# Performance work log

Hardware: AMD Instinct MI355X
Metric: run time of the kernel (lower is better)

The kernel has to match this reference:

```python
import jax, jax.numpy as jnp
import numpy as np

T, B = 256, 512
IMG_FLAT = 25          # 5*5*num_channels
FEAT = 16; LOC = 4; EMB = 4
LSTM_IN = FEAT + LOC + EMB  # 24
H = 128
GRID = 10.0


def _lin(k, out_d, in_d, scale=0.05):
    kw, kb = jax.random.split(k)
    return (jax.random.normal(kw, (out_d, in_d), jnp.float32) * scale,
            jax.random.normal(kb, (out_d,), jnp.float32) * scale)


def setup_inputs() -> dict:
    key = jax.random.key(0)
    ks = jax.random.split(key, 16)
    image = jax.random.uniform(ks[0], (T * B, 5, 5), jnp.float32) * 255.0
    location = jax.random.uniform(ks[1], (T * B, 2), jnp.float32) * GRID
    message = jax.random.normal(ks[2], (T * B, 1), jnp.float32)
    done = jax.random.randint(ks[3], (T * B,), 0, 2, jnp.int32)
    h0 = jnp.zeros((1, B, H), jnp.float32)
    c0 = jnp.zeros((1, B, H), jnp.float32)
    Wv1, bv1 = _lin(ks[4], 256, IMG_FLAT)
    Wv2, bv2 = _lin(ks[5], 256, 256)
    Wv3, bv3 = _lin(ks[6], 128, 256)
    Wv4, bv4 = _lin(ks[7], FEAT, 128)
    Wl, bl = _lin(ks[8], LOC, 2)
    Wm, bm = _lin(ks[9], EMB, 1)
    Wih, bih = _lin(ks[10], 4 * H, LSTM_IN)
    Whh, bhh = _lin(ks[11], 4 * H, H)
    return dict(image=image, location=location, message=message, done=done,
                h0=h0, c0=c0,
                Wv1=Wv1, bv1=bv1, Wv2=Wv2, bv2=bv2, Wv3=Wv3, bv3=bv3,
                Wv4=Wv4, bv4=bv4, Wl=Wl, bl=bl, Wm=Wm, bm=bm,
                Wih=Wih, bih=bih, Whh=Whh, bhh=bhh)


def _get_states(image, location, message, done_f, h0, c0,
                Wv1, bv1, Wv2, bv2, Wv3, bv3, Wv4, bv4,
                Wl, bl, Wm, bm, Wih, bih, Whh, bhh):
    batch = h0.shape[1]
    # encoders (all rows at once, faithful to torch version)
    x = image.reshape(image.shape[0], -1) / 255.0
    f = jax.nn.relu(x @ Wv1.T + bv1)
    f = jax.nn.relu(f @ Wv2.T + bv2)
    f = jax.nn.relu(f @ Wv3.T + bv3)
    image_feat = jax.nn.relu(f @ Wv4.T + bv4)                  # [TB, 16]
    loc_feat = (location / GRID) @ Wl.T + bl                    # [TB, 4]
    msg = (1.0 - done_f)[:, None] * message
    msg_feat = jax.nn.relu(msg @ Wm.T + bm)                     # [TB, 4]
    hid = jnp.concatenate([image_feat, loc_feat, msg_feat], axis=1)
    hid = hid.reshape(-1, batch, LSTM_IN)                       # [T, B, 24]
    d_seq = done_f.reshape(-1, batch)                           # [T, B]

    def step(carry, xd):
        h, c = carry
        x_t, d_t = xd
        mask = (1.0 - d_t)[:, None]
        h = h * mask
        c = c * mask
        gates = x_t @ Wih.T + bih + h @ Whh.T + bhh             # [B, 4H]
        i, fg, g, o = jnp.split(gates, 4, axis=-1)
        c = jax.nn.sigmoid(fg) * c + jax.nn.sigmoid(i) * jnp.tanh(g)
        h = jax.nn.sigmoid(o) * jnp.tanh(c)
        return (h, c), h

    (hT, cT), hs = jax.lax.scan(step, (h0[0], c0[0]), (hid, d_seq))
    new_hidden = hs.reshape(-1, H)                              # [TB, 128]
    return new_hidden, hT[None], cT[None]


def reference(image, location, message, done, h0, c0,
              Wv1, bv1, Wv2, bv2, Wv3, bv3, Wv4, bv4,
              Wl, bl, Wm, bm, Wih, bih, Whh, bhh):
    done_f = done.astype(jnp.float32)
    return _get_states(image, location, message, done_f, h0, c0,
                       Wv1, bv1, Wv2, bv2, Wv3, bv3, Wv4, bv4,
                       Wl, bl, Wm, bm, Wih, bih, Whh, bhh)
```

## Files before the change

kernel.cpp:

```cpp
#include <hip/hip_runtime.h>
#include <hip/hip_bf16.h>

#define T_STEPS 256
#define BATCH   512
#define HID     128
#define TBROWS  (T_STEPS * BATCH)
#define XH_STRIDE 32

typedef short  bh8   __attribute__((ext_vector_type(8)));
typedef _Float16 h8  __attribute__((ext_vector_type(8)));
typedef float  f32x4 __attribute__((ext_vector_type(4)));

__device__ __forceinline__ unsigned short f2bf_bits(float x) {
    union { float f; unsigned int u; } a; a.f = x;
    unsigned int r = a.u + 0x7fffu + ((a.u >> 16) & 1u);
    return (unsigned short)(r >> 16);
}
__device__ __forceinline__ unsigned short f2h_bits(float x) {
    union { _Float16 h; unsigned short u; } z; z.h = (_Float16)x; return z.u;
}
__device__ __forceinline__ unsigned int pack2h(float a, float b) {
    union { _Float16 h[2]; unsigned int u; } z;
    z.h[0] = (_Float16)a; z.h[1] = (_Float16)b; return z.u;
}

#if __has_builtin(__builtin_amdgcn_rcpf)
__device__ __forceinline__ float frcp(float x) { return __builtin_amdgcn_rcpf(x); }
#else
__device__ __forceinline__ float frcp(float x) { return 1.0f / x; }
#endif
#if __has_builtin(__builtin_amdgcn_exp2f)
__device__ __forceinline__ float fexp2(float x) { return __builtin_amdgcn_exp2f(x); }
#else
__device__ __forceinline__ float fexp2(float x) { return __expf(x * 0.6931471806f); }
#endif
#define LOG2E 1.442695041f
__device__ __forceinline__ float sigf(float x) {
    return frcp(1.0f + fexp2(-x * LOG2E));
}
__device__ __forceinline__ float tanh_fast(float x) {
    return fmaf(-2.0f, frcp(1.0f + fexp2(x * (2.0f * LOG2E))), 1.0f);
}

__device__ __forceinline__ void fragstore(unsigned short* dst, const float* W,
                                          int i, int NT, int Kreal) {
    const int j    = i & 7;
    const int lane = (i >> 3) & 63;
    const int ts   = i >> 9;
    const int nt   = ts % NT;
    const int ks   = ts / NT;
    const int n = nt * 16 + (lane & 15);
    const int k = ks * 32 + (lane >> 4) * 8 + j;
    dst[i] = (k < Kreal) ? f2bf_bits(W[n * Kreal + k]) : (unsigned short)0;
}

#define NE1 8192
#define NE2 65536
#define NE3 32768
#define NE4 2048
#define NWC 81920
#define NBS 512
#define PREP_TOTAL (NE1 + NE2 + NE3 + NE4 + NWC + NBS)

__global__ __launch_bounds__(256) void prep_kernel(
    const float* __restrict__ W1, const float* __restrict__ W2,
    const float* __restrict__ W3, const float* __restrict__ W4,
    const float* __restrict__ Wih, const float* __restrict__ bih,
    const float* __restrict__ Whh, const float* __restrict__ bhh,
    unsigned short* __restrict__ w1f, unsigned short* __restrict__ w2f,
    unsigned short* __restrict__ w3f, unsigned short* __restrict__ w4f,
    unsigned short* __restrict__ wcf, float* __restrict__ bsum)
{
    int i = blockIdx.x * 256 + threadIdx.x;
    if (i < NE1) { fragstore(w1f, W1, i, 16, 25); return; }
    i -= NE1;
    if (i < NE2) { fragstore(w2f, W2, i, 16, 256); return; }
    i -= NE2;
    if (i < NE3) { fragstore(w3f, W3, i, 8, 256); return; }
    i -= NE3;
    if (i < NE4) { fragstore(w4f, W4, i, 1, 128); return; }
    i -= NE4;
    if (i < NWC) {
        const int j    = i & 7;
        const int lane = (i >> 3) & 63;
        const int ts   = i >> 9;
        const int mt   = ts / 5;
        const int kt   = ts - mt * 5;
        const int m = mt * 16 + (lane & 15);
        const int k = kt * 32 + (lane >> 4) * 8 + j;
        float v = 0.0f;
        if (k < 128)      v = Whh[m * 128 + k];
        else if (k < 152) v = Wih[m * 24 + (k - 128)];
        wcf[i] = f2h_bits(v);
        return;
    }
    i -= NWC;
    if (i < NBS) bsum[i] = bih[i] + bhh[i];
}

#define ASTRIDE 264

__global__ __launch_bounds__(256) void encoder_kernel(
    const float* __restrict__ img,
    const float* __restrict__ loc,
    const float* __restrict__ msg,
    const int*   __restrict__ done,
    const float* __restrict__ B1, const float* __restrict__ B2,
    const float* __restrict__ B3, const float* __restrict__ B4,
    const float* __restrict__ Wl, const float* __restrict__ Bl,
    const float* __restrict__ Wm, const float* __restrict__ Bm,
    const unsigned short* __restrict__ w1f, const unsigned short* __restrict__ w2f,
    const unsigned short* __restrict__ w3f, const unsigned short* __restrict__ w4f,
    unsigned short* __restrict__ xcat_h)
{
    __shared__ unsigned short actA[4][16][ASTRIDE];
    __shared__ unsigned short actB[4][16][ASTRIDE];

    const int tid  = threadIdx.x;
    const int w    = tid >> 6;
    const int lane = tid & 63;
    const int m    = lane & 15;
    const int quad = lane >> 4;
    const int wrow0 = blockIdx.x * 64 + w * 16;

    if (tid < 64) {
        const int grow = blockIdx.x * 64 + tid;
        const float l0 = loc[grow * 2 + 0] * 0.1f;
        const float l1 = loc[grow * 2 + 1] * 0.1f;
        #pragma unroll
        for (int c = 0; c < 4; ++c)
            xcat_h[grow * XH_STRIDE + 16 + c] =
                f2h_bits(fmaf(Wl[c * 2 + 0], l0, fmaf(Wl[c * 2 + 1], l1, Bl[c])));
        const float mm = (1.0f - (float)done[grow]) * msg[grow];
        #pragma unroll
        for (int c = 0; c < 4; ++c)
            xcat_h[grow * XH_STRIDE + 20 + c] =
                f2h_bits(fmaxf(fmaf(Wm[c], mm, Bm[c]), 0.0f));
    }

    const f32x4 zero4 = {0.0f, 0.0f, 0.0f, 0.0f};

    {
        bh8 af;
        const int grow = wrow0 + m;
        #pragma unroll
        for (int j = 0; j < 8; ++j) {
            const int k = quad * 8 + j;
            const float v = (k < 25) ? img[grow * 25 + k] * (1.0f / 255.0f) : 0.0f;
            af[j] = (short)f2bf_bits(v);
        }
        f32x4 acc[16];
        #pragma unroll
        for (int nt = 0; nt < 16; ++nt) {
            const bh8 bf_ = *reinterpret_cast<const bh8*>(w1f + (nt * 64 + lane) * 8);
            acc[nt] = __builtin_amdgcn_mfma_f32_16x16x32_bf16(af, bf_, zero4, 0, 0, 0);
        }
        #pragma unroll
        for (int nt = 0; nt < 16; ++nt) {
            const float bb = B1[nt * 16 + m];
            #pragma unroll
            for (int r = 0; r < 4; ++r)
                actA[w][quad * 4 + r][nt * 16 + m] = f2bf_bits(fmaxf(acc[nt][r] + bb, 0.0f));
        }
    }

    {
        f32x4 acc[16];
        #pragma unroll
        for (int nt = 0; nt < 16; ++nt) acc[nt] = zero4;
        #pragma unroll
        for (int ks = 0; ks < 8; ++ks) {
            const bh8 af = *reinterpret_cast<const bh8*>(&actA[w][m][ks * 32 + quad * 8]);
            const unsigned short* wp = w2f + ((ks * 16) * 64 + lane) * 8;
            #pragma unroll
            for (int nt = 0; nt < 16; ++nt) {
                const bh8 bf_ = *reinterpret_cast<const bh8*>(wp + nt * 512);
                acc[nt] = __builtin_amdgcn_mfma_f32_16x16x32_bf16(af, bf_, acc[nt], 0, 0, 0);
            }
        }
        #pragma unroll
        for (int nt = 0; nt < 16; ++nt) {
            const float bb = B2[nt * 16 + m];
            #pragma unroll
            for (int r = 0; r < 4; ++r)
                actB[w][quad * 4 + r][nt * 16 + m] = f2bf_bits(fmaxf(acc[nt][r] + bb, 0.0f));
        }
    }

    {
        f32x4 acc[8];
        #pragma unroll
        for (int nt = 0; nt < 8; ++nt) acc[nt] = zero4;
        #pragma unroll
        for (int ks = 0; ks < 8; ++ks) {
            const bh8 af = *reinterpret_cast<const bh8*>(&actB[w][m][ks * 32 + quad * 8]);
            const unsigned short* wp = w3f + ((ks * 8) * 64 + lane) * 8;
            #pragma unroll
            for (int nt = 0; nt < 8; ++nt) {
                const bh8 bf_ = *reinterpret_cast<const bh8*>(wp + nt * 512);
                acc[nt] = __builtin_amdgcn_mfma_f32_16x16x32_bf16(af, bf_, acc[nt], 0, 0, 0);
            }
        }
        #pragma unroll
        for (int nt = 0; nt < 8; ++nt) {
            const float bb = B3[nt * 16 + m];
            #pragma unroll
            for (int r = 0; r < 4; ++r)
                actA[w][quad * 4 + r][nt * 16 + m] = f2bf_bits(fmaxf(acc[nt][r] + bb, 0.0f));
        }
    }

    {
        f32x4 acc = zero4;
        #pragma unroll
        for (int ks = 0; ks < 4; ++ks) {
            const bh8 af = *reinterpret_cast<const bh8*>(&actA[w][m][ks * 32 + quad * 8]);
            const bh8 bf_ = *reinterpret_cast<const bh8*>(w4f + (ks * 64 + lane) * 8);
            acc = __builtin_amdgcn_mfma_f32_16x16x32_bf16(af, bf_, acc, 0, 0, 0);
        }
        const float bb = B4[m];
        #pragma unroll
        for (int r = 0; r < 4; ++r) {
            const int grow = wrow0 + quad * 4 + r;
            xcat_h[grow * XH_STRIDE + m] = f2h_bits(fmaxf(acc[r] + bb, 0.0f));
        }
    }
}

#define HXS 168

__global__ __launch_bounds__(512, 2) void lstm_kernel(
    const unsigned short* __restrict__ xcat_h,
    const int*   __restrict__ done,
    const float* __restrict__ h0,
    const float* __restrict__ c0,
    const unsigned short* __restrict__ wcf,
    const float* __restrict__ bsum,
    float* __restrict__ out)
{
    __shared__ unsigned short hx[2][16][HXS];

    const int tid  = threadIdx.x;
    const int w    = tid >> 6;
    const int lane = tid & 63;
    const int n    = lane & 15;
    const int quad = lane >> 4;
    const int bb   = blockIdx.x * 16;
    const int u0   = w * 16 + quad * 4;

    h8 wf[4][5];
    #pragma unroll
    for (int g = 0; g < 4; ++g)
        #pragma unroll
        for (int kt = 0; kt < 5; ++kt)
            wf[g][kt] = *reinterpret_cast<const h8*>(
                wcf + (size_t)(((g * 8 + w) * 5 + kt) * 64 + lane) * 8);

    float bi[4][4];
    #pragma unroll
    for (int g = 0; g < 4; ++g)
        #pragma unroll
        for (int r = 0; r < 4; ++r)
            bi[g][r] = bsum[g * 128 + u0 + r];

    float c_[4];
    {
        const float4 cv = *reinterpret_cast<const float4*>(c0 + (size_t)(bb + n) * HID + u0);
        c_[0] = cv.x; c_[1] = cv.y; c_[2] = cv.z; c_[3] = cv.w;
    }

    if (tid < 128) {
        const int b_ = tid >> 6, r_ = (tid >> 2) & 15, j_ = tid & 3;
        *reinterpret_cast<unsigned int*>(&hx[b_][r_][152 + 2 * j_]) = 0u;
    }
    for (int i = tid; i < 16 * HID; i += 512) {
        const int nn = i >> 7, uu = i & 127;
        const float m0 = 1.0f - (float)done[bb + nn];
        hx[0][nn][uu] = f2h_bits(h0[(size_t)(bb + nn) * HID + uu] * m0);
    }
    if (tid < 192) {
        const int nl = tid / 12, kp = tid - nl * 12;
        const unsigned int v = *reinterpret_cast<const unsigned int*>(
            xcat_h + (size_t)(bb + nl) * XH_STRIDE + 2 * kp);
        *reinterpret_cast<unsigned int*>(&hx[0][nl][128 + 2 * kp]) = v;
    }
    int mc_i = done[bb + n];
    int mn_i = done[BATCH + bb + n];
    __syncthreads();

    float hn[4] = {0.0f, 0.0f, 0.0f, 0.0f};

    #pragma unroll 2
    for (int s = 0; s < T_STEPS; ++s) {
        const int buf = s & 1, nbuf = buf ^ 1;

        h8 bf[5];
        #pragma unroll
        for (int kt = 0; kt < 5; ++kt)
            bf[kt] = *reinterpret_cast<const h8*>(&hx[buf][n][kt * 32 + quad * 8]);

        unsigned int xreg = 0;
        if (tid < 192) {
            const int nl = tid / 12, kp = tid - nl * 12;
            const int rowx = (s + 1 < T_STEPS ? s + 1 : T_STEPS - 1) * BATCH + bb + nl;
            xreg = *reinterpret_cast<const unsigned int*>(
                xcat_h + (size_t)rowx * XH_STRIDE + 2 * kp);
        }
        const int mf_i = done[(s + 2 < T_STEPS ? s + 2 : T_STEPS - 1) * BATCH + bb + n];

        f32x4 acc[4];
        #pragma unroll
        for (int g = 0; g < 4; ++g) {
            acc[g][0] = bi[g][0]; acc[g][1] = bi[g][1];
            acc[g][2] = bi[g][2]; acc[g][3] = bi[g][3];
        }
        #pragma unroll
        for (int kt = 0; kt < 5; ++kt)
            #pragma unroll
            for (int g = 0; g < 4; ++g)
                acc[g] = __builtin_amdgcn_mfma_f32_16x16x32_f16(wf[g][kt], bf[kt], acc[g], 0, 0, 0);

        const float mcur = 1.0f - (float)mc_i;
        const float mnxt = 1.0f - (float)mn_i;
        #pragma unroll
        for (int r = 0; r < 4; ++r) {
            const float gi = acc[0][r], gf = acc[1][r];
            const float gg = acc[2][r], go = acc[3][r];
            const float cn = sigf(gf) * (c_[r] * mcur) + sigf(gi) * tanh_fast(gg);
            hn[r] = sigf(go) * tanh_fast(cn);
            c_[r] = cn;
        }

        const int row = s * BATCH + bb + n;
        float4 ov; ov.x = hn[0]; ov.y = hn[1]; ov.z = hn[2]; ov.w = hn[3];
        *reinterpret_cast<float4*>(out + (size_t)row * HID + u0) = ov;

        *reinterpret_cast<unsigned int*>(&hx[nbuf][n][u0])     = pack2h(hn[0] * mnxt, hn[1] * mnxt);
        *reinterpret_cast<unsigned int*>(&hx[nbuf][n][u0 + 2]) = pack2h(hn[2] * mnxt, hn[3] * mnxt);
        if (tid < 192) {
            const int nl = tid / 12, kp = tid - nl * 12;
            *reinterpret_cast<unsigned int*>(&hx[nbuf][nl][128 + 2 * kp]) = xreg;
        }
        mc_i = mn_i; mn_i = mf_i;
        __syncthreads();
    }

    const size_t base = (size_t)TBROWS * HID;
    float4 hv; hv.x = hn[0]; hv.y = hn[1]; hv.z = hn[2]; hv.w = hn[3];
    *reinterpret_cast<float4*>(out + base + (size_t)(bb + n) * HID + u0) = hv;
    float4 cvo; cvo.x = c_[0]; cvo.y = c_[1]; cvo.z = c_[2]; cvo.w = c_[3];
    *reinterpret_cast<float4*>(out + base + (size_t)BATCH * HID + (size_t)(bb + n) * HID + u0) = cvo;
}

extern "C" void kernel_launch(void* const* d_in, const int* in_sizes, int n_in,
                              void* d_out, int out_size, void* d_ws, size_t ws_size,
                              hipStream_t stream) {
    const float* img  = (const float*)d_in[0];
    const float* loc  = (const float*)d_in[1];
    const float* msg  = (const float*)d_in[2];
    const int*   done = (const int*)d_in[3];
    const float* h0   = (const float*)d_in[4];
    const float* c0   = (const float*)d_in[5];
    const float* W1   = (const float*)d_in[6];
    const float* B1   = (const float*)d_in[7];
    const float* W2   = (const float*)d_in[8];
    const float* B2   = (const float*)d_in[9];
    const float* W3   = (const float*)d_in[10];
    const float* B3   = (const float*)d_in[11];
    const float* W4   = (const float*)d_in[12];
    const float* B4   = (const float*)d_in[13];
    const float* Wl   = (const float*)d_in[14];
    const float* Bl   = (const float*)d_in[15];
    const float* Wm   = (const float*)d_in[16];
    const float* Bm   = (const float*)d_in[17];
    const float* Wih  = (const float*)d_in[18];
    const float* bih  = (const float*)d_in[19];
    const float* Whh  = (const float*)d_in[20];
    const float* bhh  = (const float*)d_in[21];

    char* wsb = (char*)d_ws;
    unsigned short* xcat_h = (unsigned short*)wsb;
    unsigned short* w1f = (unsigned short*)(wsb + (size_t)TBROWS * XH_STRIDE * 2);
    unsigned short* w2f = w1f + NE1;
    unsigned short* w3f = w2f + NE2;
    unsigned short* w4f = w3f + NE3;
    unsigned short* wcf = w4f + NE4;
    float*          bsum = (float*)(wcf + NWC);

    float* out = (float*)d_out;

    prep_kernel<<<(PREP_TOTAL + 255) / 256, 256, 0, stream>>>(
        W1, W2, W3, W4, Wih, bih, Whh, bhh,
        w1f, w2f, w3f, w4f, wcf, bsum);
    encoder_kernel<<<TBROWS / 64, 256, 0, stream>>>(
        img, loc, msg, done, B1, B2, B3, B4, Wl, Bl, Wm, Bm,
        w1f, w2f, w3f, w4f, xcat_h);
    lstm_kernel<<<BATCH / 16, 512, 0, stream>>>(
        xcat_h, done, h0, c0, wcf, bsum, out);
}
```

Baseline: 413.3 us.

## Transpose encoder MFMAs to 32 rows per wave and split LSTM into 2-column blocks

```diff
diff --git a/kernel.cpp b/kernel.cpp
--- a/kernel.cpp
+++ b/kernel.cpp
@@ -22,6 +22,9 @@
 __device__ __forceinline__ unsigned int pack2h(float a, float b) {
     union { _Float16 h[2]; unsigned int u; } z;
     z.h[0] = (_Float16)a; z.h[1] = (_Float16)b; return z.u;
+}
+__device__ __forceinline__ unsigned int pack2bf(float a, float b) {
+    return (unsigned int)f2bf_bits(a) | ((unsigned int)f2bf_bits(b) << 16);
 }
 
 #if __has_builtin(__builtin_amdgcn_rcpf)
@@ -113,123 +116,160 @@
     const unsigned short* __restrict__ w3f, const unsigned short* __restrict__ w4f,
     unsigned short* __restrict__ xcat_h)
 {
-    __shared__ unsigned short actA[4][16][ASTRIDE];
-    __shared__ unsigned short actB[4][16][ASTRIDE];
+    __shared__ __align__(16) unsigned short actA[4][32][ASTRIDE];
+    __shared__ __align__(16) unsigned short actB[4][32][ASTRIDE];
 
     const int tid  = threadIdx.x;
     const int w    = tid >> 6;
     const int lane = tid & 63;
-    const int m    = lane & 15;
+    const int n    = lane & 15;
     const int quad = lane >> 4;
-    const int wrow0 = blockIdx.x * 64 + w * 16;
-
-    if (tid < 64) {
-        const int grow = blockIdx.x * 64 + tid;
-        const float l0 = loc[grow * 2 + 0] * 0.1f;
-        const float l1 = loc[grow * 2 + 1] * 0.1f;
+    const int wrow0 = blockIdx.x * 128 + w * 32;
+
+    if (tid < 128) {
+        const int grow = blockIdx.x * 128 + tid;
+        const float l0 = loc[(size_t)grow * 2 + 0] * 0.1f;
+        const float l1 = loc[(size_t)grow * 2 + 1] * 0.1f;
         #pragma unroll
         for (int c = 0; c < 4; ++c)
-            xcat_h[grow * XH_STRIDE + 16 + c] =
+            xcat_h[(size_t)grow * XH_STRIDE + 16 + c] =
                 f2h_bits(fmaf(Wl[c * 2 + 0], l0, fmaf(Wl[c * 2 + 1], l1, Bl[c])));
         const float mm = (1.0f - (float)done[grow]) * msg[grow];
         #pragma unroll
         for (int c = 0; c < 4; ++c)
-            xcat_h[grow * XH_STRIDE + 20 + c] =
+            xcat_h[(size_t)grow * XH_STRIDE + 20 + c] =
                 f2h_bits(fmaxf(fmaf(Wm[c], mm, Bm[c]), 0.0f));
     }
 
     const f32x4 zero4 = {0.0f, 0.0f, 0.0f, 0.0f};
 
     {
-        bh8 af;
-        const int grow = wrow0 + m;
-        #pragma unroll
-        for (int j = 0; j < 8; ++j) {
-            const int k = quad * 8 + j;
-            const float v = (k < 25) ? img[grow * 25 + k] * (1.0f / 255.0f) : 0.0f;
-            af[j] = (short)f2bf_bits(v);
-        }
-        f32x4 acc[16];
-        #pragma unroll
-        for (int nt = 0; nt < 16; ++nt) {
-            const bh8 bf_ = *reinterpret_cast<const bh8*>(w1f + (nt * 64 + lane) * 8);
-            acc[nt] = __builtin_amdgcn_mfma_f32_16x16x32_bf16(af, bf_, zero4, 0, 0, 0);
-        }
-        #pragma unroll
-        for (int nt = 0; nt < 16; ++nt) {
-            const float bb = B1[nt * 16 + m];
-            #pragma unroll
-            for (int r = 0; r < 4; ++r)
-                actA[w][quad * 4 + r][nt * 16 + m] = f2bf_bits(fmaxf(acc[nt][r] + bb, 0.0f));
-        }
-    }
+        bh8 bimg[2];
+        #pragma unroll
+        for (int sg = 0; sg < 2; ++sg) {
+            const size_t grow = wrow0 + sg * 16 + n;
+            #pragma unroll
+            for (int j = 0; j < 8; ++j) {
+                const int k = quad * 8 + j;
+                const float v = (k < 25) ? img[grow * 25 + k] * (1.0f / 255.0f) : 0.0f;
+                bimg[sg][j] = (short)f2bf_bits(v);
+            }
+        }
+        f32x4 a1[16][2];
+        #pragma unroll
+        for (int mt = 0; mt < 16; ++mt) {
+            const bh8 a = *reinterpret_cast<const bh8*>(w1f + (size_t)(mt * 64 + lane) * 8);
+            a1[mt][0] = __builtin_amdgcn_mfma_f32_16x16x32_bf16(a, bimg[0], zero4, 0, 0, 0);
+            a1[mt][1] = __builtin_amdgcn_mfma_f32_16x16x32_bf16(a, bimg[1], zero4, 0, 0, 0);
+        }
+        #pragma unroll
+        for (int mt = 0; mt < 16; ++mt) {
+            const float4 bv = *reinterpret_cast<const float4*>(B1 + mt * 16 + quad * 4);
+            #pragma unroll
+            for (int sg = 0; sg < 2; ++sg) {
+                const float v0 = fmaxf(a1[mt][sg][0] + bv.x, 0.0f);
+                const float v1 = fmaxf(a1[mt][sg][1] + bv.y, 0.0f);
+                const float v2 = fmaxf(a1[mt][sg][2] + bv.z, 0.0f);
+                const float v3 = fmaxf(a1[mt][sg][3] + bv.w, 0.0f);
+                uint2 pk; pk.x = pack2bf(v0, v1); pk.y = pack2bf(v2, v3);
+                *reinterpret_cast<uint2*>(&actA[w][sg * 16 + n][mt * 16 + quad * 4]) = pk;
+            }
+        }
+    }
+    __syncthreads();
 
     {
-        f32x4 acc[16];
-        #pragma unroll
-        for (int nt = 0; nt < 16; ++nt) acc[nt] = zero4;
-        #pragma unroll
-        for (int ks = 0; ks < 8; ++ks) {
-            const bh8 af = *reinterpret_cast<const bh8*>(&actA[w][m][ks * 32 + quad * 8]);
-            const unsigned short* wp = w2f + ((ks * 16) * 64 + lane) * 8;
-            #pragma unroll
-            for (int nt = 0; nt < 16; ++nt) {
-                const bh8 bf_ = *reinterpret_cast<const bh8*>(wp + nt * 512);
-                acc[nt] = __builtin_amdgcn_mfma_f32_16x16x32_bf16(af, bf_, acc[nt], 0, 0, 0);
-            }
-        }
-        #pragma unroll
-        for (int nt = 0; nt < 16; ++nt) {
-            const float bb = B2[nt * 16 + m];
-            #pragma unroll
-            for (int r = 0; r < 4; ++r)
-                actB[w][quad * 4 + r][nt * 16 + m] = f2bf_bits(fmaxf(acc[nt][r] + bb, 0.0f));
-        }
-    }
+        f32x4 a2[16][2];
+        #pragma unroll
+        for (int mt = 0; mt < 16; ++mt) { a2[mt][0] = zero4; a2[mt][1] = zero4; }
+        #pragma unroll
+        for (int kt = 0; kt < 8; ++kt) {
+            const bh8 b0 = *reinterpret_cast<const bh8*>(&actA[w][n][kt * 32 + quad * 8]);
+            const bh8 b1 = *reinterpret_cast<const bh8*>(&actA[w][16 + n][kt * 32 + quad * 8]);
+            #pragma unroll
+            for (int mt = 0; mt < 16; ++mt) {
+                const bh8 a = *reinterpret_cast<const bh8*>(
+                    w2f + (size_t)((kt * 16 + mt) * 64 + lane) * 8);
+                a2[mt][0] = __builtin_amdgcn_mfma_f32_16x16x32_bf16(a, b0, a2[mt][0], 0, 0, 0);
+                a2[mt][1] = __builtin_amdgcn_mfma_f32_16x16x32_bf16(a, b1, a2[mt][1], 0, 0, 0);
+            }
+        }
+        #pragma unroll
+        for (int mt = 0; mt < 16; ++mt) {
+            const float4 bv = *reinterpret_cast<const float4*>(B2 + mt * 16 + quad * 4);
+            #pragma unroll
+            for (int sg = 0; sg < 2; ++sg) {
+                const float v0 = fmaxf(a2[mt][sg][0] + bv.x, 0.0f);
+                const float v1 = fmaxf(a2[mt][sg][1] + bv.y, 0.0f);
+                const float v2 = fmaxf(a2[mt][sg][2] + bv.z, 0.0f);
+                const float v3 = fmaxf(a2[mt][sg][3] + bv.w, 0.0f);
+                uint2 pk; pk.x = pack2bf(v0, v1); pk.y = pack2bf(v2, v3);
+                *reinterpret_cast<uint2*>(&actB[w][sg * 16 + n][mt * 16 + quad * 4]) = pk;
+            }
+        }
+    }
+    __syncthreads();
 
     {
-        f32x4 acc[8];
-        #pragma unroll
-        for (int nt = 0; nt < 8; ++nt) acc[nt] = zero4;
-        #pragma unroll
-        for (int ks = 0; ks < 8; ++ks) {
-            const bh8 af = *reinterpret_cast<const bh8*>(&actB[w][m][ks * 32 + quad * 8]);
-            const unsigned short* wp = w3f + ((ks * 8) * 64 + lane) * 8;
-            #pragma unroll
-            for (int nt = 0; nt < 8; ++nt) {
-                const bh8 bf_ = *reinterpret_cast<const bh8*>(wp + nt * 512);
-                acc[nt] = __builtin_amdgcn_mfma_f32_16x16x32_bf16(af, bf_, acc[nt], 0, 0, 0);
-            }
-        }
-        #pragma unroll
-        for (int nt = 0; nt < 8; ++nt) {
-            const float bb = B3[nt * 16 + m];
-            #pragma unroll
-            for (int r = 0; r < 4; ++r)
-                actA[w][quad * 4 + r][nt * 16 + m] = f2bf_bits(fmaxf(acc[nt][r] + bb, 0.0f));
-        }
-    }
+        f32x4 a3[8][2];
+        #pragma unroll
+        for (int mt = 0; mt < 8; ++mt) { a3[mt][0] = zero4; a3[mt][1] = zero4; }
+        #pragma unroll
+        for (int kt = 0; kt < 8; ++kt) {
+            const bh8 b0 = *reinterpret_cast<const bh8*>(&actB[w][n][kt * 32 + quad * 8]);
+            const bh8 b1 = *reinterpret_cast<const bh8*>(&actB[w][16 + n][kt * 32 + quad * 8]);
+            #pragma unroll
+            for (int mt = 0; mt < 8; ++mt) {
+                const bh8 a = *reinterpret_cast<const bh8*>(
+                    w3f + (size_t)((kt * 8 + mt) * 64 + lane) * 8);
+                a3[mt][0] = __builtin_amdgcn_mfma_f32_16x16x32_bf16(a, b0, a3[mt][0], 0, 0, 0);
+                a3[mt][1] = __builtin_amdgcn_mfma_f32_16x16x32_bf16(a, b1, a3[mt][1], 0, 0, 0);
+            }
+        }
+        #pragma unroll
+        for (int mt = 0; mt < 8; ++mt) {
+            const float4 bv = *reinterpret_cast<const float4*>(B3 + mt * 16 + quad * 4);
+            #pragma unroll
+            for (int sg = 0; sg < 2; ++sg) {
+                const float v0 = fmaxf(a3[mt][sg][0] + bv.x, 0.0f);
+                const float v1 = fmaxf(a3[mt][sg][1] + bv.y, 0.0f);
+                const float v2 = fmaxf(a3[mt][sg][2] + bv.z, 0.0f);
+                const float v3 = fmaxf(a3[mt][sg][3] + bv.w, 0.0f);
+                uint2 pk; pk.x = pack2bf(v0, v1); pk.y = pack2bf(v2, v3);
+                *reinterpret_cast<uint2*>(&actA[w][sg * 16 + n][mt * 16 + quad * 4]) = pk;
+            }
+        }
+    }
+    __syncthreads();
 
     {
-        f32x4 acc = zero4;
-        #pragma unroll
-        for (int ks = 0; ks < 4; ++ks) {
-            const bh8 af = *reinterpret_cast<const bh8*>(&actA[w][m][ks * 32 + quad * 8]);
-            const bh8 bf_ = *reinterpret_cast<const bh8*>(w4f + (ks * 64 + lane) * 8);
-            acc = __builtin_amdgcn_mfma_f32_16x16x32_bf16(af, bf_, acc, 0, 0, 0);
-        }
-        const float bb = B4[m];
-        #pragma unroll
-        for (int r = 0; r < 4; ++r) {
-            const int grow = wrow0 + quad * 4 + r;
-            xcat_h[grow * XH_STRIDE + m] = f2h_bits(fmaxf(acc[r] + bb, 0.0f));
-        }
-    }
-}
-
+        f32x4 a4[2] = {zero4, zero4};
+        #pragma unroll
+        for (int kt = 0; kt < 4; ++kt) {
+            const bh8 b0 = *reinterpret_cast<const bh8*>(&actA[w][n][kt * 32 + quad * 8]);
+            const bh8 b1 = *reinterpret_cast<const bh8*>(&actA[w][16 + n][kt * 32 + quad * 8]);
+            const bh8 a = *reinterpret_cast<const bh8*>(w4f + (size_t)(kt * 64 + lane) * 8);
+            a4[0] = __builtin_amdgcn_mfma_f32_16x16x32_bf16(a, b0, a4[0], 0, 0, 0);
+            a4[1] = __builtin_amdgcn_mfma_f32_16x16x32_bf16(a, b1, a4[1], 0, 0, 0);
+        }
+        const float4 bv = *reinterpret_cast<const float4*>(B4 + quad * 4);
+        #pragma unroll
+        for (int sg = 0; sg < 2; ++sg) {
+            const int grow = wrow0 + sg * 16 + n;
+            const float v0 = fmaxf(a4[sg][0] + bv.x, 0.0f);
+            const float v1 = fmaxf(a4[sg][1] + bv.y, 0.0f);
+            const float v2 = fmaxf(a4[sg][2] + bv.z, 0.0f);
+            const float v3 = fmaxf(a4[sg][3] + bv.w, 0.0f);
+            uint2 pk; pk.x = pack2h(v0, v1); pk.y = pack2h(v2, v3);
+            *reinterpret_cast<uint2*>(xcat_h + (size_t)grow * XH_STRIDE + quad * 4) = pk;
+        }
+    }
+}
+
+#define COLS 2
 #define HXS 168
 
-__global__ __launch_bounds__(512, 2) void lstm_kernel(
+__global__ __launch_bounds__(256) void lstm_kernel(
     const unsigned short* __restrict__ xcat_h,
     const int*   __restrict__ done,
     const float* __restrict__ h0,
@@ -238,61 +278,55 @@
     const float* __restrict__ bsum,
     float* __restrict__ out)
 {
-    __shared__ unsigned short hx[2][16][HXS];
+    __shared__ __align__(16) unsigned short hx[2][16][HXS];
+    __shared__ __align__(16) float gbuf[COLS][130][4];
 
     const int tid  = threadIdx.x;
     const int w    = tid >> 6;
     const int lane = tid & 63;
     const int n    = lane & 15;
     const int quad = lane >> 4;
-    const int bb   = blockIdx.x * 16;
-    const int u0   = w * 16 + quad * 4;
-
-    h8 wf[4][5];
+    const int bb   = blockIdx.x * COLS;
+
+    h8 wf[2][4][5];
     #pragma unroll
-    for (int g = 0; g < 4; ++g)
-        #pragma unroll
-        for (int kt = 0; kt < 5; ++kt)
-            wf[g][kt] = *reinterpret_cast<const h8*>(
-                wcf + (size_t)(((g * 8 + w) * 5 + kt) * 64 + lane) * 8);
-
-    float bi[4][4];
+    for (int h = 0; h < 2; ++h)
+        #pragma unroll
+        for (int g = 0; g < 4; ++g)
+            #pragma unroll
+            for (int kt = 0; kt < 5; ++kt)
+                wf[h][g][kt] = *reinterpret_cast<const h8*>(
+                    wcf + (size_t)(((g * 8 + w + 4 * h) * 5 + kt) * 64 + lane) * 8);
+
+    const int tn = tid >> 7;
+    const int tu = tid & 127;
+    float bi_t[4];
     #pragma unroll
-    for (int g = 0; g < 4; ++g)
-        #pragma unroll
-        for (int r = 0; r < 4; ++r)
-            bi[g][r] = bsum[g * 128 + u0 + r];
-
-    float c_[4];
-    {
-        const float4 cv = *reinterpret_cast<const float4*>(c0 + (size_t)(bb + n) * HID + u0);
-        c_[0] = cv.x; c_[1] = cv.y; c_[2] = cv.z; c_[3] = cv.w;
-    }
-
-    if (tid < 128) {
-        const int b_ = tid >> 6, r_ = (tid >> 2) & 15, j_ = tid & 3;
-        *reinterpret_cast<unsigned int*>(&hx[b_][r_][152 + 2 * j_]) = 0u;
-    }
-    for (int i = tid; i < 16 * HID; i += 512) {
-        const int nn = i >> 7, uu = i & 127;
-        const float m0 = 1.0f - (float)done[bb + nn];
-        hx[0][nn][uu] = f2h_bits(h0[(size_t)(bb + nn) * HID + uu] * m0);
-    }
-    if (tid < 192) {
+    for (int g = 0; g < 4; ++g) bi_t[g] = bsum[g * 128 + tu];
+
+    float c_ = c0[(size_t)(bb + tn) * HID + tu];
+    const float h0v = h0[(size_t)(bb + tn) * HID + tu];
+
+    for (int i = tid; i < 2 * 16 * HXS / 2; i += 256)
+        reinterpret_cast<unsigned int*>(hx)[i] = 0u;
+    __syncthreads();
+
+    int mc = done[bb + tn];
+    int mn = done[BATCH + bb + tn];
+    hx[0][tn][tu] = f2h_bits(h0v * (1.0f - (float)mc));
+    if (tid < COLS * 12) {
         const int nl = tid / 12, kp = tid - nl * 12;
-        const unsigned int v = *reinterpret_cast<const unsigned int*>(
-            xcat_h + (size_t)(bb + nl) * XH_STRIDE + 2 * kp);
-        *reinterpret_cast<unsigned int*>(&hx[0][nl][128 + 2 * kp]) = v;
-    }
-    int mc_i = done[bb + n];
-    int mn_i = done[BATCH + bb + n];
+        *reinterpret_cast<unsigned int*>(&hx[0][nl][128 + 2 * kp]) =
+            *reinterpret_cast<const unsigned int*>(
+                xcat_h + (size_t)(bb + nl) * XH_STRIDE + 2 * kp);
+    }
     __syncthreads();
 
-    float hn[4] = {0.0f, 0.0f, 0.0f, 0.0f};
-
-    #pragma unroll 2
+    float hl = 0.0f;
+
+    #pragma unroll 1
     for (int s = 0; s < T_STEPS; ++s) {
-        const int buf = s & 1, nbuf = buf ^ 1;
+        const int buf = s & 1;
 
         h8 bf[5];
         #pragma unroll
@@ -300,56 +334,68 @@
             bf[kt] = *reinterpret_cast<const h8*>(&hx[buf][n][kt * 32 + quad * 8]);
 
         unsigned int xreg = 0;
-        if (tid < 192) {
+        if (tid < COLS * 12) {
             const int nl = tid / 12, kp = tid - nl * 12;
             const int rowx = (s + 1 < T_STEPS ? s + 1 : T_STEPS - 1) * BATCH + bb + nl;
             xreg = *reinterpret_cast<const unsigned int*>(
                 xcat_h + (size_t)rowx * XH_STRIDE + 2 * kp);
         }
-        const int mf_i = done[(s + 2 < T_STEPS ? s + 2 : T_STEPS - 1) * BATCH + bb + n];
-
-        f32x4 acc[4];
-        #pragma unroll
-        for (int g = 0; g < 4; ++g) {
-            acc[g][0] = bi[g][0]; acc[g][1] = bi[g][1];
-            acc[g][2] = bi[g][2]; acc[g][3] = bi[g][3];
-        }
+        const int mf = done[(s + 2 < T_STEPS ? s + 2 : T_STEPS - 1) * BATCH + bb + tn];
+
+        f32x4 acc[2][4];
+        #pragma unroll
+        for (int h = 0; h < 2; ++h)
+            #pragma unroll
+            for (int g = 0; g < 4; ++g) acc[h][g] = (f32x4){0.0f, 0.0f, 0.0f, 0.0f};
         #pragma unroll
         for (int kt = 0; kt < 5; ++kt)
             #pragma unroll
-            for (int g = 0; g < 4; ++g)
-                acc[g] = __builtin_amdgcn_mfma_f32_16x16x32_f16(wf[g][kt], bf[kt], acc[g], 0, 0, 0);
-
-        const float mcur = 1.0f - (float)mc_i;
-        const float mnxt = 1.0f - (float)mn_i;
-        #pragma unroll
-        for (int r = 0; r < 4; ++r) {
-            const float gi = acc[0][r], gf = acc[1][r];
-            const float gg = acc[2][r], go = acc[3][r];
-            const float cn = sigf(gf) * (c_[r] * mcur) + sigf(gi) * tanh_fast(gg);
-            hn[r] = sigf(go) * tanh_fast(cn);
-            c_[r] = cn;
-        }
-
-        const int row = s * BATCH + bb + n;
-        float4 ov; ov.x = hn[0]; ov.y = hn[1]; ov.z = hn[2]; ov.w = hn[3];
-        *reinterpret_cast<float4*>(out + (size_t)row * HID + u0) = ov;
-
-        *reinterpret_cast<unsigned int*>(&hx[nbuf][n][u0])     = pack2h(hn[0] * mnxt, hn[1] * mnxt);
-        *reinterpret_cast<unsigned int*>(&hx[nbuf][n][u0 + 2]) = pack2h(hn[2] * mnxt, hn[3] * mnxt);
-        if (tid < 192) {
+            for (int h = 0; h < 2; ++h)
+                #pragma unroll
+                for (int g = 0; g < 4; ++g)
+                    acc[h][g] = __builtin_amdgcn_mfma_f32_16x16x32_f16(
+                        wf[h][g][kt], bf[kt], acc[h][g], 0, 0, 0);
+
+        if (n < COLS) {
+            #pragma unroll
+            for (int h = 0; h < 2; ++h) {
+                const int ub = (w + 4 * h) * 16 + quad * 4;
+                #pragma unroll
+                for (int r = 0; r < 4; ++r) {
+                    float4 gv;
+                    gv.x = acc[h][0][r]; gv.y = acc[h][1][r];
+                    gv.z = acc[h][2][r]; gv.w = acc[h][3][r];
+                    *reinterpret_cast<float4*>(&gbuf[n][ub + r][0]) = gv;
+                }
+            }
+        }
+        __syncthreads();
+
+        const float4 gv = *reinterpret_cast<const float4*>(&gbuf[tn][tu][0]);
+        const float mcur = 1.0f - (float)mc;
+        const float mnxt = 1.0f - (float)mn;
+        const float gi = gv.x + bi_t[0];
+        const float gf = gv.y + bi_t[1];
+        const float gg = gv.z + bi_t[2];
+        const float go = gv.w + bi_t[3];
+        const float cn = sigf(gf) * (c_ * mcur) + sigf(gi) * tanh_fast(gg);
+        const float hn = sigf(go) * tanh_fast(cn);
+        c_ = cn; hl = hn;
+
+        const int row = s * BATCH + bb + tn;
+        out[(size_t)row * HID + tu] = hn;
+        hx[buf ^ 1][tn][tu] = f2h_bits(hn * mnxt);
+        if (tid < COLS * 12) {
             const int nl = tid / 12, kp = tid - nl * 12;
-            *reinterpret_cast<unsigned int*>(&hx[nbuf][nl][128 + 2 * kp]) = xreg;
-        }
-        mc_i = mn_i; mn_i = mf_i;
+            *reinterpret_cast<unsigned int*>(&hx[buf ^ 1][nl][128 + 2 * kp]) = xreg;
+        }
+        mc = mn; mn = mf;
         __syncthreads();
     }
 
     const size_t base = (size_t)TBROWS * HID;
-    float4 hv; hv.x = hn[0]; hv.y = hn[1]; hv.z = hn[2]; hv.w = hn[3];
-    *reinterpret_cast<float4*>(out + base + (size_t)(bb + n) * HID + u0) = hv;
-    float4 cvo; cvo.x = c_[0]; cvo.y = c_[1]; cvo.z = c_[2]; cvo.w = c_[3];
-    *reinterpret_cast<float4*>(out + base + (size_t)BATCH * HID + (size_t)(bb + n) * HID + u0) = cvo;
+    out[base + (size_t)(bb + tn) * HID + tu] = hl;
+    out[base + (size_t)BATCH * HID + (size_t)(bb + tn) * HID + tu] = c_;
 }
 
 extern "C" void kernel_launch(void* const* d_in, const int* in_sizes, int n_in,
@@ -392,9 +438,9 @@
     prep_kernel<<<(PREP_TOTAL + 255) / 256, 256, 0, stream>>>(
         W1, W2, W3, W4, Wih, bih, Whh, bhh,
         w1f, w2f, w3f, w4f, wcf, bsum);
-    encoder_kernel<<<TBROWS / 64, 256, 0, stream>>>(
+    encoder_kernel<<<TBROWS / 128, 256, 0, stream>>>(
         img, loc, msg, done, B1, B2, B3, B4, Wl, Bl, Wm, Bm,
         w1f, w2f, w3f, w4f, xcat_h);
-    lstm_kernel<<<BATCH / 16, 512, 0, stream>>>(
+    lstm_kernel<<<BATCH / COLS, 256, 0, stream>>>(
         xcat_h, done, h0, c0, wcf, bsum, out);
 }
```

Result: faster. 402.8 us (-2.5%).
